# Kernel tuning notes

Measured on AMD Instinct MI355X. Metric: run time of the kernel, lower is better.

The kernel has to match this reference:

```python
import jax, jax.numpy as jnp
import numpy as np

N = 100_000   # nodes
E = 1_600_000 # edges
F_IN = 128
H = 128
C = 16


def setup_inputs() -> dict:
    key = jax.random.key(0)
    ks = jax.random.split(key, 11)
    s = 0.05
    return {
        "x": jax.random.normal(ks[0], (N, F_IN), jnp.float32),
        "edge_index": jax.random.randint(ks[1], (2, E), 0, N, jnp.int32),
        "edge_weight": jax.random.uniform(ks[2], (E,), jnp.float32),
        # first_lin: Linear(features_num, hidden)
        "W_first": jax.random.normal(ks[3], (F_IN, H), jnp.float32) * s,
        "b_first": jax.random.normal(ks[4], (H,), jnp.float32) * s,
        # two GCNConv(hidden, hidden) layers (num_layers - 1 = 2)
        "W_conv1": jax.random.normal(ks[5], (H, H), jnp.float32) * s,
        "b_conv1": jax.random.normal(ks[6], (H,), jnp.float32) * s,
        "W_conv2": jax.random.normal(ks[7], (H, H), jnp.float32) * s,
        "b_conv2": jax.random.normal(ks[8], (H,), jnp.float32) * s,
        # lin2: Linear(hidden, num_class)
        "W_out": jax.random.normal(ks[9], (H, C), jnp.float32) * s,
        "b_out": jax.random.normal(ks[10], (C,), jnp.float32) * s,
    }


def reference(x, edge_index, edge_weight, W_first, b_first,
              W_conv1, b_conv1, W_conv2, b_conv2, W_out, b_out):
    src, dst = edge_index[0], edge_index[1]

    # first_lin + relu (dropout p=0.8 is identity at inference)
    h = jax.nn.relu(x @ W_first + b_first)

    # GCN normalization with self-loops (fill weight 1.0), shared across layers
    deg = jax.ops.segment_sum(edge_weight, dst, num_segments=N) + 1.0
    dinv = jax.lax.rsqrt(deg)                      # [N]
    norm = dinv[src] * edge_weight * dinv[dst]     # [E]
    self_norm = dinv * dinv                        # [N], self-loop contribution

    for W, b in ((W_conv1, b_conv1), (W_conv2, b_conv2)):
        hw = h @ W                                  # [N, H]
        msgs = hw[src] * norm[:, None]              # [E, H] gather + scale
        agg = jax.ops.segment_sum(msgs, dst, num_segments=N)
        agg = agg + hw * self_norm[:, None]         # self-loop term
        h = jax.nn.relu(agg + b)

    # dropout p=0.5 identity at inference; final linear
    return h @ W_out + b_out
```

## Files before the change

### kernel.cpp

```cpp
#include <hip/hip_runtime.h>

typedef unsigned short u16;
typedef unsigned int u32;
using bf16x8 = __attribute__((ext_vector_type(8))) short;
using f32x4  = __attribute__((ext_vector_type(4))) float;

#define SLOT 64
#define RNG 16
#define SPR 4
#define NSHARD 16
#define LDSN 6250
#define CB 256
#define OVF_CAP 65536

static __device__ __forceinline__ u16 f2bf(float f) {
    u32 u = __float_as_uint(f);
    u = (u + 0x7fffu + ((u >> 16) & 1u)) >> 16;
    return (u16)u;
}
static __device__ __forceinline__ float bf2f(u16 h) {
    return __uint_as_float(((u32)h) << 16);
}
static __device__ __forceinline__ float pk_w(u32 e) {
    return (float)(int)((e & 0x7fffu) - 1u) * (1.0f / 32766.0f);
}

__global__ __launch_bounds__(256) void k_part1(const int* __restrict__ dst,
                                               int* __restrict__ cnt, int E, int CH) {
    __shared__ int lc[NSHARD];
    if (threadIdx.x < NSHARD) lc[threadIdx.x] = 0;
    __syncthreads();
    int e0 = blockIdx.x * CH, e1 = min(E, e0 + CH);
    for (int e = e0 + (int)threadIdx.x; e < e1; e += 256)
        atomicAdd(&lc[dst[e] & (NSHARD - 1)], 1);
    __syncthreads();
    if (threadIdx.x < NSHARD) cnt[blockIdx.x * NSHARD + threadIdx.x] = lc[threadIdx.x];
}

__global__ __launch_bounds__(256) void k_scan(const int* __restrict__ cnt,
                                              int* __restrict__ offs, int E) {
    __shared__ int sd[256];
    int t = threadIdx.x;
    int carry = 0;
    for (int base = 0; base < NSHARD * CB; base += 256) {
        int idx = base + t;
        int s = idx / CB, b = idx % CB;
        int v = cnt[b * NSHARD + s];
        sd[t] = v;
        __syncthreads();
        for (int off = 1; off < 256; off <<= 1) {
            int x = (t >= off) ? sd[t - off] : 0;
            __syncthreads();
            sd[t] += x;
            __syncthreads();
        }
        offs[idx] = sd[t] - v + carry;
        carry += sd[255];
        __syncthreads();
    }
    if (t == 0) offs[NSHARD * CB] = E;
}

__global__ __launch_bounds__(256) void k_part2(
    const int* __restrict__ src, const int* __restrict__ dst,
    const float* __restrict__ ew, const int* __restrict__ offs,
    int2* __restrict__ part, int E, int CH) {
    __shared__ int base[NSHARD];
    int t = threadIdx.x, b = blockIdx.x;
    if (t < NSHARD) base[t] = offs[t * CB + b];
    __syncthreads();
    int e0 = b * CH, e1 = min(E, e0 + CH);
    for (int e = e0 + t; e < e1; e += 256) {
        int d = dst[e];
        int s = d & (NSHARD - 1);
        float w = ew[e];
        u32 w15 = 1u + (u32)fminf(w * 32766.0f + 0.5f, 32766.0f);
        u32 ent = ((u32)src[e] << 15) | w15;
        int pos = atomicAdd(&base[s], 1);
        part[pos] = make_int2(d, (int)ent);
    }
}

static __device__ __forceinline__ void fill2_body(
    u32* __restrict__ lcur, int fb, const int2* __restrict__ part,
    const int* __restrict__ offs, u32* __restrict__ bucket,
    int2* __restrict__ ovf, int* __restrict__ ovf_cnt, int E) {
    const int s = fb & (NSHARD - 1);
    const int r = fb >> 4;
    for (int i = threadIdx.x; i < LDSN; i += 256) lcur[i] = 0;
    __syncthreads();
    const int sb = offs[s * CB];
    const int se = offs[(s + 1) * CB];
    const int sz = se - sb;
    const int CHS = (sz + RNG - 1) / RNG;
    const int e0 = sb + r * CHS, e1 = min(se, e0 + CHS);
    for (int e = e0 + (int)threadIdx.x; e < e1; e += 256) {
        int2 v = part[e];
        int d = v.x;
        int ln = d >> 4;
        u32 p = atomicAdd(&lcur[ln], 1u);
        if (p < SPR) {
            bucket[(size_t)d * SLOT + r * SPR + p] = (u32)v.y;
        } else {
            int g = atomicAdd(ovf_cnt, 1);
            if (g < OVF_CAP) ovf[g] = v;
        }
    }
}

__global__ void k_fixup(u32* __restrict__ bucket, const int2* __restrict__ ovf,
                        const int* __restrict__ ovf_cnt) {
    int i = blockIdx.x * blockDim.x + threadIdx.x;
    int c = min(*ovf_cnt, OVF_CAP);
    if (i >= c) return;
    int2 v = ovf[i];
    u32* bp = bucket + (size_t)v.x * SLOT;
    for (int k = 0; k < SLOT; ++k) {
        if (bp[k] == 0u) {
            if (atomicCAS(&bp[k], 0u, (u32)v.y) == 0u) return;
        }
    }
}

static __device__ __forceinline__ void dinv_body(
    const u32* __restrict__ bucket, float* __restrict__ dinv, int n, int db)
{
    int node = db * 16 + (threadIdx.x >> 4);
    if (node >= n) return;
    int l = threadIdx.x & 15;
    const u32* bp = bucket + (size_t)node * SLOT;
    float sum = 0.f;
#pragma unroll
    for (int k = 0; k < 4; ++k) {
        u32 e = bp[l + k * 16];
        if (e) sum += pk_w(e);
    }
    sum += __shfl_xor(sum, 1);
    sum += __shfl_xor(sum, 2);
    sum += __shfl_xor(sum, 4);
    sum += __shfl_xor(sum, 8);
    if (l == 0) dinv[node] = rsqrtf(1.0f + sum);
}

template <bool AF32, bool RELU_BIAS>
static __device__ __forceinline__ void gemm_body(
    u16* __restrict__ Wf, int bid, const void* __restrict__ Araw,
    const float* __restrict__ W, const float* __restrict__ bias,
    u16* __restrict__ C, int n)
{
    const int t = threadIdx.x;
#pragma unroll
    for (int it = 0; it < 8; ++it) {
        int fid = it * 256 + t;
        int c  = fid & 15;
        int g  = (fid >> 4) & 3;
        int kk = (fid >> 6) & 3;
        int ct = fid >> 8;
        int col = ct * 16 + c;
        int k0 = kk * 32 + g * 8;
        const float* wp = W + (size_t)k0 * 128 + col;
        bf16x8 pv;
#pragma unroll
        for (int j = 0; j < 8; ++j) pv[j] = (short)f2bf(wp[(size_t)j * 128]);
        *(bf16x8*)&Wf[(size_t)fid * 8] = pv;
    }
    __syncthreads();

    const int lane = t & 63;
    const int wave = t >> 6;
    const int rowbase = bid * 128 + wave * 32;
    const int lrow = lane & 15;
    const int g = lane >> 4;

    bf16x8 a[2][4];
#pragma unroll
    for (int rt = 0; rt < 2; ++rt) {
        int r = rowbase + rt * 16 + lrow;
        if (r < n) {
            if (AF32) {
                const float* ap = (const float*)Araw + (size_t)r * 128 + g * 8;
#pragma unroll
                for (int kki = 0; kki < 4; ++kki) {
                    float4 v0 = *(const float4*)(ap + kki * 32);
                    float4 v1 = *(const float4*)(ap + kki * 32 + 4);
                    bf16x8 av;
                    av[0] = (short)f2bf(v0.x);
                    av[1] = (short)f2bf(v0.y);
                    av[2] = (short)f2bf(v0.z);
                    av[3] = (short)f2bf(v0.w);
                    av[4] = (short)f2bf(v1.x);
                    av[5] = (short)f2bf(v1.y);
                    av[6] = (short)f2bf(v1.z);
                    av[7] = (short)f2bf(v1.w);
                    a[rt][kki] = av;
                }
            } else {
                const u16* ap = (const u16*)Araw + (size_t)r * 128 + g * 8;
#pragma unroll
                for (int kki = 0; kki < 4; ++kki)
                    a[rt][kki] = *(const bf16x8*)(ap + kki * 32);
            }
        } else {
#pragma unroll
            for (int kki = 0; kki < 4; ++kki)
                a[rt][kki] = (bf16x8)(short)0;
        }
    }

    f32x4 acc[2][8];
#pragma unroll
    for (int rt = 0; rt < 2; ++rt)
#pragma unroll
        for (int ct = 0; ct < 8; ++ct)
            acc[rt][ct] = (f32x4)0.0f;

#pragma unroll
    for (int ct = 0; ct < 8; ++ct) {
#pragma unroll
        for (int kki = 0; kki < 4; ++kki) {
            bf16x8 b = *(const bf16x8*)&Wf[((size_t)(ct * 4 + kki) * 64 + lane) * 8];
            acc[0][ct] = __builtin_amdgcn_mfma_f32_16x16x32_bf16(a[0][kki], b, acc[0][ct], 0, 0, 0);
            acc[1][ct] = __builtin_amdgcn_mfma_f32_16x16x32_bf16(a[1][kki], b, acc[1][ct], 0, 0, 0);
        }
    }

#pragma unroll
    for (int rt = 0; rt < 2; ++rt) {
#pragma unroll
        for (int ct = 0; ct < 8; ++ct) {
            int c = ct * 16 + lrow;
            float bv = 0.f;
            if (RELU_BIAS) bv = bias[c];
#pragma unroll
            for (int j = 0; j < 4; ++j) {
                int r = rowbase + rt * 16 + g * 4 + j;
                if (r < n) {
                    float v = acc[rt][ct][j];
                    if (RELU_BIAS) v = fmaxf(v + bv, 0.f);
                    C[(size_t)r * 128 + c] = f2bf(v);
                }
            }
        }
    }
}

__global__ __launch_bounds__(256) void kC(
    const int2* __restrict__ part, const int* __restrict__ offs,
    u32* __restrict__ bucket, int2* __restrict__ ovf, int* __restrict__ ovf_cnt,
    int E,
    const float* __restrict__ x, const float* __restrict__ W,
    const float* __restrict__ bias, u16* __restrict__ C, int n)
{
    __shared__ u16 Wf[2048 * 8];
    if ((int)blockIdx.x < NSHARD * RNG)
        fill2_body((u32*)Wf, blockIdx.x, part, offs, bucket, ovf, ovf_cnt, E);
    else
        gemm_body<true, true>(Wf, blockIdx.x - NSHARD * RNG, x, W, bias, C, n);
}

__global__ __launch_bounds__(256) void kB(
    const u16* __restrict__ A, const float* __restrict__ W,
    u16* __restrict__ C, int n, int G,
    const u32* __restrict__ bucket, float* __restrict__ dinv)
{
    __shared__ u16 Wf[2048 * 8];
    if ((int)blockIdx.x < G)
        gemm_body<false, false>(Wf, blockIdx.x, A, W, nullptr, C, n);
    else
        dinv_body(bucket, dinv, n, blockIdx.x - G);
}

__global__ __launch_bounds__(256) void k_gemm(
    const u16* __restrict__ A, const float* __restrict__ W,
    u16* __restrict__ C, int n)
{
    __shared__ u16 Wf[2048 * 8];
    gemm_body<false, false>(Wf, blockIdx.x, A, W, nullptr, C, n);
}

__global__ __launch_bounds__(256) void k_gather_fin(
    const u16* __restrict__ hw, const u32* __restrict__ bucket,
    const float* __restrict__ dinv, const float* __restrict__ bias,
    u16* __restrict__ hout, int n)
{
    __shared__ u32 comp[4][64];
    const int w = threadIdx.x >> 6;
    const int lane = threadIdx.x & 63;
    const int node = blockIdx.x * 4 + w;
    const bool active = node < n;

    u32 ent = 0;
    if (active) ent = bucket[(size_t)node * SLOT + lane];
    unsigned long long mask = __ballot(ent != 0);
    int nv = __popcll(mask);
    int pos = __popcll(mask & ((1ull << lane) - 1ull));
    if (ent) comp[w][pos] = ent;
    __syncthreads();
    if (!active) return;

    const int grp = lane >> 4;
    const int gl = lane & 15;
    float acc[8] = {0.f, 0.f, 0.f, 0.f, 0.f, 0.f, 0.f, 0.f};
    int nit = (nv + 3) >> 2;
    int it = 0;
    for (; it + 1 < nit; it += 2) {
        int ka = it * 4 + grp;
        int kb = ka + 4;
        bool vb = kb < nv;
        u32 ea = comp[w][ka];
        u32 eb = comp[w][vb ? kb : 0];
        int sa = (int)(ea >> 15), sb = (int)(eb >> 15);
        bf16x8 ra = *(const bf16x8*)(hw + (size_t)sa * 128 + gl * 8);
        bf16x8 rb = *(const bf16x8*)(hw + (size_t)sb * 128 + gl * 8);
        float wa = dinv[sa] * pk_w(ea);
        float wb = vb ? dinv[sb] * pk_w(eb) : 0.f;
#pragma unroll
        for (int j = 0; j < 8; ++j) acc[j] = fmaf(wa, bf2f((u16)ra[j]), acc[j]);
#pragma unroll
        for (int j = 0; j < 8; ++j) acc[j] = fmaf(wb, bf2f((u16)rb[j]), acc[j]);
    }
    if (it < nit) {
        int ka = it * 4 + grp;
        bool va = ka < nv;
        u32 ea = comp[w][va ? ka : 0];
        int sa = (int)(ea >> 15);
        bf16x8 ra = *(const bf16x8*)(hw + (size_t)sa * 128 + gl * 8);
        float wa = va ? dinv[sa] * pk_w(ea) : 0.f;
#pragma unroll
        for (int j = 0; j < 8; ++j) acc[j] = fmaf(wa, bf2f((u16)ra[j]), acc[j]);
    }
#pragma unroll
    for (int j = 0; j < 8; ++j) {
        acc[j] += __shfl_xor(acc[j], 16);
        acc[j] += __shfl_xor(acc[j], 32);
    }
    if (grp == 0) {
        float di = dinv[node];
        bf16x8 srow = *(const bf16x8*)(hw + (size_t)node * 128 + gl * 8);
        float4 b0 = *(const float4*)(bias + gl * 8);
        float4 b1 = *(const float4*)(bias + gl * 8 + 4);
        float bv[8] = {b0.x, b0.y, b0.z, b0.w, b1.x, b1.y, b1.z, b1.w};
        bf16x8 po;
#pragma unroll
        for (int j = 0; j < 8; ++j) {
            float val = fmaf(di, fmaf(di, bf2f((u16)srow[j]), acc[j]), bv[j]);
            po[j] = (short)f2bf(fmaxf(val, 0.f));
        }
        *(bf16x8*)(hout + (size_t)node * 128 + gl * 8) = po;
    }
}

__global__ void k_gemm_out(const u16* __restrict__ h, const float* __restrict__ W,
                           const float* __restrict__ bias, float* __restrict__ out, int n) {
    __shared__ float hs[16][132];
    __shared__ float wsT[16][132];
    __shared__ float bs[16];
    int t = threadIdx.x;
    int row0 = blockIdx.x * 16;
    int r = t >> 4, c = t & 15;
    {
        int gr = row0 + r;
        if (gr < n) {
            const u16* hp = h + (size_t)gr * 128 + c * 8;
            ushort4 v0 = *(const ushort4*)(hp);
            ushort4 v1 = *(const ushort4*)(hp + 4);
            hs[r][c * 8 + 0] = bf2f(v0.x);
            hs[r][c * 8 + 1] = bf2f(v0.y);
            hs[r][c * 8 + 2] = bf2f(v0.z);
            hs[r][c * 8 + 3] = bf2f(v0.w);
            hs[r][c * 8 + 4] = bf2f(v1.x);
            hs[r][c * 8 + 5] = bf2f(v1.y);
            hs[r][c * 8 + 6] = bf2f(v1.z);
            hs[r][c * 8 + 7] = bf2f(v1.w);
        } else {
#pragma unroll
            for (int j = 0; j < 8; ++j) hs[r][c * 8 + j] = 0.f;
        }
    }
#pragma unroll
    for (int j = 0; j < 8; ++j) {
        int idx = t * 8 + j;
        int k = idx >> 4, cc = idx & 15;
        wsT[cc][k] = W[idx];
    }
    if (t < 16) bs[t] = bias[t];
    __syncthreads();
    float acc = 0.f;
#pragma unroll
    for (int k = 0; k < 128; k += 4) {
        float4 a = *(const float4*)&hs[r][k];
        float4 b = *(const float4*)&wsT[c][k];
        acc += a.x * b.x + a.y * b.y + a.z * b.z + a.w * b.w;
    }
    int gr = row0 + r;
    if (gr < n) out[gr * 16 + c] = acc + bs[c];
}

extern "C" void kernel_launch(void* const* d_in, const int* in_sizes, int n_in,
                              void* d_out, int out_size, void* d_ws, size_t ws_size,
                              hipStream_t stream) {
    const float* x  = (const float*)d_in[0];
    const int*   ei = (const int*)d_in[1];
    const float* ew = (const float*)d_in[2];
    const float* Wf = (const float*)d_in[3];
    const float* bf = (const float*)d_in[4];
    const float* W1 = (const float*)d_in[5];
    const float* b1 = (const float*)d_in[6];
    const float* W2 = (const float*)d_in[7];
    const float* b2 = (const float*)d_in[8];
    const float* Wo = (const float*)d_in[9];
    const float* bo = (const float*)d_in[10];
    float* out = (float*)d_out;

    const int N = in_sizes[0] / 128;
    const int E = in_sizes[2];
    const int* src = ei;
    const int* dst = ei + E;

    char* ws = (char*)d_ws;
    size_t off = 0;
    auto alloc = [&](size_t bytes) -> void* {
        void* p = ws + off;
        off = (off + bytes + 255) & ~(size_t)255;
        return p;
    };
    float* dinv    = (float*)alloc((size_t)N * 4);
    int*   ovf_cnt = (int*)alloc(256);
    int2*  ovf     = (int2*)alloc((size_t)OVF_CAP * 8);
    int*   cnt     = (int*)alloc((size_t)CB * NSHARD * 4);
    int*   offs    = (int*)alloc(((size_t)CB * NSHARD + 1) * 4);
    int2*  part    = (int2*)alloc((size_t)E * 8);
    u32*   bucket  = (u32*)alloc((size_t)N * SLOT * 4);
    u16*   bufA    = (u16*)alloc((size_t)N * 128 * 2);
    u16*   bufB    = (u16*)alloc((size_t)N * 128 * 2);
    (void)ws_size; (void)n_in; (void)out_size;

    const int G  = (N + 127) / 128;
    const int Db = (N + 15) / 16;
    const int gat_grid = (N + 3) / 4;
    const int CH = (E + CB - 1) / CB;

    hipMemsetAsync(bucket, 0, (size_t)N * SLOT * 4, stream);
    hipMemsetAsync(ovf_cnt, 0, 4, stream);

    k_part1<<<CB, 256, 0, stream>>>(dst, cnt, E, CH);
    k_scan<<<1, 256, 0, stream>>>(cnt, offs, E);
    k_part2<<<CB, 256, 0, stream>>>(src, dst, ew, offs, part, E, CH);

    kC<<<NSHARD * RNG + G, 256, 0, stream>>>(part, offs, bucket, ovf, ovf_cnt, E,
                                             x, Wf, bf, bufA, N);
    k_fixup<<<OVF_CAP / 256, 256, 0, stream>>>(bucket, ovf, ovf_cnt);

    kB<<<G + Db, 256, 0, stream>>>(bufA, W1, bufB, N, G, bucket, dinv);
    k_gather_fin<<<gat_grid, 256, 0, stream>>>(bufB, bucket, dinv, b1, bufA, N);
    k_gemm<<<G, 256, 0, stream>>>(bufA, W2, bufB, N);
    k_gather_fin<<<gat_grid, 256, 0, stream>>>(bufB, bucket, dinv, b2, bufA, N);
    k_gemm_out<<<(N + 15) / 16, 256, 0, stream>>>(bufA, Wo, bo, out, N);
}
```

Before: 316.1 us.

## Restructure edge bucketing into LDS-staged shards and fuse output linear into gather

Edge partitioning now uses 128 shards with a two-level parallel scan instead of a single-block scan. Each fill block stages the slot lists in LDS and writes them out as coalesced uint4 stores, which removes the bucket memset and the scattered global writes. The destination shard pass is merged with the first GEMM, and weight fragments are precomputed once in a prep kernel instead of inside every GEMM block. The final 128x16 linear is fused into the second gather kernel, dropping a kernel launch and one full round trip of the hidden activations. The costs are larger LDS use per fill block, a padded bucket layout, and more overflow entries when a node receives more than 16 edges in one quarter.

Result: faster. 269.9 us (-14.6%).

```diff
diff --git a/kernel.cpp b/kernel.cpp
--- a/kernel.cpp
+++ b/kernel.cpp
@@ -6,12 +6,14 @@
 using f32x4  = __attribute__((ext_vector_type(4))) float;
 
 #define SLOT 64
-#define RNG 16
-#define SPR 4
-#define NSHARD 16
-#define LDSN 6250
+#define NSHARD 128
+#define SHMASK 127
+#define SHBITS 7
+#define QRT 4
+#define SPQ 16
+#define LDSN 782
 #define CB 256
-#define OVF_CAP 65536
+#define OVF_CAP 131072
 
 static __device__ __forceinline__ u16 f2bf(float f) {
     u32 u = __float_as_uint(f);
@@ -24,148 +26,77 @@
 static __device__ __forceinline__ float pk_w(u32 e) {
     return (float)(int)((e & 0x7fffu) - 1u) * (1.0f / 32766.0f);
 }
+static __device__ __forceinline__ size_t nodeBase(int d) {
+    return ((size_t)((d & SHMASK) * LDSN + (d >> SHBITS))) << 6;
+}
+
+__global__ void k_prep(const float* __restrict__ Wf, const float* __restrict__ W1,
+                       const float* __restrict__ W2, u16* __restrict__ wfrag) {
+    const float* W = (blockIdx.x == 0) ? Wf : (blockIdx.x == 1 ? W1 : W2);
+    u16* o = wfrag + (size_t)blockIdx.x * 16384;
+    for (int fid = threadIdx.x; fid < 2048; fid += 256) {
+        int c = fid & 15, g = (fid >> 4) & 3, kk = (fid >> 6) & 3, ct = fid >> 8;
+        const float* wp = W + (size_t)(kk * 32 + g * 8) * 128 + ct * 16 + c;
+        bf16x8 pv;
+#pragma unroll
+        for (int j = 0; j < 8; ++j) pv[j] = (short)f2bf(wp[(size_t)j * 128]);
+        *(bf16x8*)&o[(size_t)fid * 8] = pv;
+    }
+}
 
 __global__ __launch_bounds__(256) void k_part1(const int* __restrict__ dst,
                                                int* __restrict__ cnt, int E, int CH) {
     __shared__ int lc[NSHARD];
-    if (threadIdx.x < NSHARD) lc[threadIdx.x] = 0;
+    for (int i = threadIdx.x; i < NSHARD; i += 256) lc[i] = 0;
     __syncthreads();
     int e0 = blockIdx.x * CH, e1 = min(E, e0 + CH);
     for (int e = e0 + (int)threadIdx.x; e < e1; e += 256)
-        atomicAdd(&lc[dst[e] & (NSHARD - 1)], 1);
-    __syncthreads();
-    if (threadIdx.x < NSHARD) cnt[blockIdx.x * NSHARD + threadIdx.x] = lc[threadIdx.x];
-}
-
-__global__ __launch_bounds__(256) void k_scan(const int* __restrict__ cnt,
-                                              int* __restrict__ offs, int E) {
+        atomicAdd(&lc[dst[e] & SHMASK], 1);
+    __syncthreads();
+    for (int i = threadIdx.x; i < NSHARD; i += 256)
+        cnt[blockIdx.x * NSHARD + i] = lc[i];
+}
+
+__global__ __launch_bounds__(256) void k_scan_a(const int* __restrict__ cnt,
+                                                int* __restrict__ offs,
+                                                int* __restrict__ tot) {
     __shared__ int sd[256];
+    int s = blockIdx.x, t = threadIdx.x;
+    int v = cnt[t * NSHARD + s];
+    sd[t] = v;
+    __syncthreads();
+    for (int off = 1; off < 256; off <<= 1) {
+        int x = (t >= off) ? sd[t - off] : 0;
+        __syncthreads();
+        sd[t] += x;
+        __syncthreads();
+    }
+    offs[s * CB + t] = sd[t] - v;
+    if (t == 255) tot[s] = sd[255];
+}
+
+__global__ void k_scan_b(const int* __restrict__ tot, int* __restrict__ base, int E) {
+    __shared__ int sd[NSHARD];
     int t = threadIdx.x;
-    int carry = 0;
-    for (int base = 0; base < NSHARD * CB; base += 256) {
-        int idx = base + t;
-        int s = idx / CB, b = idx % CB;
-        int v = cnt[b * NSHARD + s];
-        sd[t] = v;
+    int v = tot[t];
+    sd[t] = v;
+    __syncthreads();
+    for (int off = 1; off < NSHARD; off <<= 1) {
+        int x = (t >= off) ? sd[t - off] : 0;
         __syncthreads();
-        for (int off = 1; off < 256; off <<= 1) {
-            int x = (t >= off) ? sd[t - off] : 0;
-            __syncthreads();
-            sd[t] += x;
-            __syncthreads();
-        }
-        offs[idx] = sd[t] - v + carry;
-        carry += sd[255];
+        sd[t] += x;
         __syncthreads();
     }
-    if (t == 0) offs[NSHARD * CB] = E;
-}
-
-__global__ __launch_bounds__(256) void k_part2(
-    const int* __restrict__ src, const int* __restrict__ dst,
-    const float* __restrict__ ew, const int* __restrict__ offs,
-    int2* __restrict__ part, int E, int CH) {
-    __shared__ int base[NSHARD];
-    int t = threadIdx.x, b = blockIdx.x;
-    if (t < NSHARD) base[t] = offs[t * CB + b];
-    __syncthreads();
-    int e0 = b * CH, e1 = min(E, e0 + CH);
-    for (int e = e0 + t; e < e1; e += 256) {
-        int d = dst[e];
-        int s = d & (NSHARD - 1);
-        float w = ew[e];
-        u32 w15 = 1u + (u32)fminf(w * 32766.0f + 0.5f, 32766.0f);
-        u32 ent = ((u32)src[e] << 15) | w15;
-        int pos = atomicAdd(&base[s], 1);
-        part[pos] = make_int2(d, (int)ent);
-    }
-}
-
-static __device__ __forceinline__ void fill2_body(
-    u32* __restrict__ lcur, int fb, const int2* __restrict__ part,
-    const int* __restrict__ offs, u32* __restrict__ bucket,
-    int2* __restrict__ ovf, int* __restrict__ ovf_cnt, int E) {
-    const int s = fb & (NSHARD - 1);
-    const int r = fb >> 4;
-    for (int i = threadIdx.x; i < LDSN; i += 256) lcur[i] = 0;
-    __syncthreads();
-    const int sb = offs[s * CB];
-    const int se = offs[(s + 1) * CB];
-    const int sz = se - sb;
-    const int CHS = (sz + RNG - 1) / RNG;
-    const int e0 = sb + r * CHS, e1 = min(se, e0 + CHS);
-    for (int e = e0 + (int)threadIdx.x; e < e1; e += 256) {
-        int2 v = part[e];
-        int d = v.x;
-        int ln = d >> 4;
-        u32 p = atomicAdd(&lcur[ln], 1u);
-        if (p < SPR) {
-            bucket[(size_t)d * SLOT + r * SPR + p] = (u32)v.y;
-        } else {
-            int g = atomicAdd(ovf_cnt, 1);
-            if (g < OVF_CAP) ovf[g] = v;
-        }
-    }
-}
-
-__global__ void k_fixup(u32* __restrict__ bucket, const int2* __restrict__ ovf,
-                        const int* __restrict__ ovf_cnt) {
-    int i = blockIdx.x * blockDim.x + threadIdx.x;
-    int c = min(*ovf_cnt, OVF_CAP);
-    if (i >= c) return;
-    int2 v = ovf[i];
-    u32* bp = bucket + (size_t)v.x * SLOT;
-    for (int k = 0; k < SLOT; ++k) {
-        if (bp[k] == 0u) {
-            if (atomicCAS(&bp[k], 0u, (u32)v.y) == 0u) return;
-        }
-    }
-}
-
-static __device__ __forceinline__ void dinv_body(
-    const u32* __restrict__ bucket, float* __restrict__ dinv, int n, int db)
-{
-    int node = db * 16 + (threadIdx.x >> 4);
-    if (node >= n) return;
-    int l = threadIdx.x & 15;
-    const u32* bp = bucket + (size_t)node * SLOT;
-    float sum = 0.f;
-#pragma unroll
-    for (int k = 0; k < 4; ++k) {
-        u32 e = bp[l + k * 16];
-        if (e) sum += pk_w(e);
-    }
-    sum += __shfl_xor(sum, 1);
-    sum += __shfl_xor(sum, 2);
-    sum += __shfl_xor(sum, 4);
-    sum += __shfl_xor(sum, 8);
-    if (l == 0) dinv[node] = rsqrtf(1.0f + sum);
+    base[t] = sd[t] - v;
+    if (t == NSHARD - 1) base[NSHARD] = E;
 }
 
 template <bool AF32, bool RELU_BIAS>
 static __device__ __forceinline__ void gemm_body(
-    u16* __restrict__ Wf, int bid, const void* __restrict__ Araw,
-    const float* __restrict__ W, const float* __restrict__ bias,
-    u16* __restrict__ C, int n)
+    int bid, const void* __restrict__ Araw, const u16* __restrict__ Wfrag,
+    const float* __restrict__ bias, u16* __restrict__ C, int n)
 {
     const int t = threadIdx.x;
-#pragma unroll
-    for (int it = 0; it < 8; ++it) {
-        int fid = it * 256 + t;
-        int c  = fid & 15;
-        int g  = (fid >> 4) & 3;
-        int kk = (fid >> 6) & 3;
-        int ct = fid >> 8;
-        int col = ct * 16 + c;
-        int k0 = kk * 32 + g * 8;
-        const float* wp = W + (size_t)k0 * 128 + col;
-        bf16x8 pv;
-#pragma unroll
-        for (int j = 0; j < 8; ++j) pv[j] = (short)f2bf(wp[(size_t)j * 128]);
-        *(bf16x8*)&Wf[(size_t)fid * 8] = pv;
-    }
-    __syncthreads();
-
     const int lane = t & 63;
     const int wave = t >> 6;
     const int rowbase = bid * 128 + wave * 32;
@@ -218,7 +149,7 @@
     for (int ct = 0; ct < 8; ++ct) {
 #pragma unroll
         for (int kki = 0; kki < 4; ++kki) {
-            bf16x8 b = *(const bf16x8*)&Wf[((size_t)(ct * 4 + kki) * 64 + lane) * 8];
+            bf16x8 b = *(const bf16x8*)&Wfrag[((size_t)(ct * 4 + kki) * 64 + lane) * 8];
             acc[0][ct] = __builtin_amdgcn_mfma_f32_16x16x32_bf16(a[0][kki], b, acc[0][ct], 0, 0, 0);
             acc[1][ct] = __builtin_amdgcn_mfma_f32_16x16x32_bf16(a[1][kki], b, acc[1][ct], 0, 0, 0);
         }
@@ -244,53 +175,144 @@
     }
 }
 
-__global__ __launch_bounds__(256) void kC(
-    const int2* __restrict__ part, const int* __restrict__ offs,
+__global__ __launch_bounds__(256) void kD(
+    const int* __restrict__ src, const int* __restrict__ dst,
+    const float* __restrict__ ew, const int* __restrict__ offs,
+    const int* __restrict__ base, int2* __restrict__ part, int E, int CH,
+    const float* __restrict__ x, const u16* __restrict__ wfragF,
+    const float* __restrict__ bias, u16* __restrict__ C, int n)
+{
+    __shared__ int sbase[NSHARD];
+    if ((int)blockIdx.x < CB) {
+        int b = blockIdx.x, t = threadIdx.x;
+        for (int i = t; i < NSHARD; i += 256) sbase[i] = base[i] + offs[i * CB + b];
+        __syncthreads();
+        int e0 = b * CH, e1 = min(E, e0 + CH);
+        for (int e = e0 + t; e < e1; e += 256) {
+            int d = dst[e];
+            float w = ew[e];
+            u32 w15 = 1u + (u32)fminf(w * 32766.0f + 0.5f, 32766.0f);
+            u32 ent = ((u32)src[e] << 15) | w15;
+            int pos = atomicAdd(&sbase[d & SHMASK], 1);
+            part[pos] = make_int2(d, (int)ent);
+        }
+    } else {
+        gemm_body<true, true>(blockIdx.x - CB, x, wfragF, bias, C, n);
+    }
+}
+
+__global__ __launch_bounds__(256) void k_fill3(
+    const int2* __restrict__ part, const int* __restrict__ base,
     u32* __restrict__ bucket, int2* __restrict__ ovf, int* __restrict__ ovf_cnt,
-    int E,
-    const float* __restrict__ x, const float* __restrict__ W,
-    const float* __restrict__ bias, u16* __restrict__ C, int n)
-{
-    __shared__ u16 Wf[2048 * 8];
-    if ((int)blockIdx.x < NSHARD * RNG)
-        fill2_body((u32*)Wf, blockIdx.x, part, offs, bucket, ovf, ovf_cnt, E);
-    else
-        gemm_body<true, true>(Wf, blockIdx.x - NSHARD * RNG, x, W, bias, C, n);
+    int n)
+{
+    __shared__ u32 slots[LDSN * SPQ];
+    __shared__ u32 cur[LDSN];
+    const int s = blockIdx.x >> 2;
+    const int q = blockIdx.x & 3;
+    for (int i = threadIdx.x; i < LDSN * SPQ; i += 256) slots[i] = 0;
+    for (int i = threadIdx.x; i < LDSN; i += 256) cur[i] = 0;
+    __syncthreads();
+    const int rb = base[s], re = base[s + 1];
+    const int CHS = (re - rb + 3) >> 2;
+    const int e0 = rb + q * CHS, e1 = min(re, e0 + CHS);
+    for (int e = e0 + (int)threadIdx.x; e < e1; e += 256) {
+        int2 v = part[e];
+        int ln = v.x >> SHBITS;
+        u32 p = atomicAdd(&cur[ln], 1u);
+        if (p < SPQ) {
+            slots[ln * SPQ + p] = (u32)v.y;
+        } else {
+            int g2 = atomicAdd(ovf_cnt, 1);
+            if (g2 < OVF_CAP) ovf[g2] = v;
+        }
+    }
+    __syncthreads();
+    for (int i = threadIdx.x; i < LDSN * 4; i += 256) {
+        int ln = i >> 2, k = i & 3;
+        int d = (ln << SHBITS) + s;
+        if (d < n) {
+            u32* dp = bucket + nodeBase(d) + q * SPQ + k * 4;
+            *(uint4*)dp = *(const uint4*)&slots[ln * SPQ + k * 4];
+        }
+    }
+}
+
+__global__ void k_fixup(u32* __restrict__ bucket, const int2* __restrict__ ovf,
+                        const int* __restrict__ ovf_cnt) {
+    int i = blockIdx.x * blockDim.x + threadIdx.x;
+    int c = min(*ovf_cnt, OVF_CAP);
+    if (i >= c) return;
+    int2 v = ovf[i];
+    u32* bp = bucket + nodeBase(v.x);
+    for (int k = 0; k < SLOT; ++k) {
+        if (bp[k] == 0u) {
+            if (atomicCAS(&bp[k], 0u, (u32)v.y) == 0u) return;
+        }
+    }
+}
+
+static __device__ __forceinline__ void dinv_body(
+    const u32* __restrict__ bucket, float* __restrict__ dinv, int n, int db)
+{
+    int node = db * 16 + (threadIdx.x >> 4);
+    if (node >= n) return;
+    int l = threadIdx.x & 15;
+    const u32* bp = bucket + nodeBase(node);
+    float sum = 0.f;
+#pragma unroll
+    for (int k = 0; k < 4; ++k) {
+        u32 e = bp[l + k * 16];
+        if (e) sum += pk_w(e);
+    }
+    sum += __shfl_xor(sum, 1);
+    sum += __shfl_xor(sum, 2);
+    sum += __shfl_xor(sum, 4);
+    sum += __shfl_xor(sum, 8);
+    if (l == 0) dinv[node] = rsqrtf(1.0f + sum);
 }
 
 __global__ __launch_bounds__(256) void kB(
-    const u16* __restrict__ A, const float* __restrict__ W,
+    const u16* __restrict__ A, const u16* __restrict__ wfrag1,
     u16* __restrict__ C, int n, int G,
     const u32* __restrict__ bucket, float* __restrict__ dinv)
 {
-    __shared__ u16 Wf[2048 * 8];
     if ((int)blockIdx.x < G)
-        gemm_body<false, false>(Wf, blockIdx.x, A, W, nullptr, C, n);
+        gemm_body<false, false>(blockIdx.x, A, wfrag1, nullptr, C, n);
     else
         dinv_body(bucket, dinv, n, blockIdx.x - G);
 }
 
 __global__ __launch_bounds__(256) void k_gemm(
-    const u16* __restrict__ A, const float* __restrict__ W,
+    const u16* __restrict__ A, const u16* __restrict__ wfrag,
     u16* __restrict__ C, int n)
 {
-    __shared__ u16 Wf[2048 * 8];
-    gemm_body<false, false>(Wf, blockIdx.x, A, W, nullptr, C, n);
-}
-
+    gemm_body<false, false>(blockIdx.x, A, wfrag, nullptr, C, n);
+}
+
+template <bool FINAL>
 __global__ __launch_bounds__(256) void k_gather_fin(
     const u16* __restrict__ hw, const u32* __restrict__ bucket,
     const float* __restrict__ dinv, const float* __restrict__ bias,
-    u16* __restrict__ hout, int n)
+    u16* __restrict__ hout,
+    const float* __restrict__ Wo, const float* __restrict__ bo,
+    float* __restrict__ out, int n)
 {
     __shared__ u32 comp[4][64];
+    __shared__ float WoS[FINAL ? 2048 : 1];
+    __shared__ float bos[FINAL ? 16 : 1];
     const int w = threadIdx.x >> 6;
     const int lane = threadIdx.x & 63;
     const int node = blockIdx.x * 4 + w;
     const bool active = node < n;
 
+    if (FINAL) {
+        for (int i = threadIdx.x; i < 2048; i += 256) WoS[i] = Wo[i];
+        if (threadIdx.x < 16) bos[threadIdx.x] = bo[threadIdx.x];
+    }
+
     u32 ent = 0;
-    if (active) ent = bucket[(size_t)node * SLOT + lane];
+    if (active) ent = bucket[nodeBase(node) + lane];
     unsigned long long mask = __ballot(ent != 0);
     int nv = __popcll(mask);
     int pos = __popcll(mask & ((1ull << lane) - 1ull));
@@ -334,66 +356,36 @@
         acc[j] += __shfl_xor(acc[j], 16);
         acc[j] += __shfl_xor(acc[j], 32);
     }
-    if (grp == 0) {
-        float di = dinv[node];
-        bf16x8 srow = *(const bf16x8*)(hw + (size_t)node * 128 + gl * 8);
-        float4 b0 = *(const float4*)(bias + gl * 8);
-        float4 b1 = *(const float4*)(bias + gl * 8 + 4);
-        float bv[8] = {b0.x, b0.y, b0.z, b0.w, b1.x, b1.y, b1.z, b1.w};
-        bf16x8 po;
-#pragma unroll
-        for (int j = 0; j < 8; ++j) {
-            float val = fmaf(di, fmaf(di, bf2f((u16)srow[j]), acc[j]), bv[j]);
-            po[j] = (short)f2bf(fmaxf(val, 0.f));
-        }
-        *(bf16x8*)(hout + (size_t)node * 128 + gl * 8) = po;
-    }
-}
-
-__global__ void k_gemm_out(const u16* __restrict__ h, const float* __restrict__ W,
-                           const float* __restrict__ bias, float* __restrict__ out, int n) {
-    __shared__ float hs[16][132];
-    __shared__ float wsT[16][132];
-    __shared__ float bs[16];
-    int t = threadIdx.x;
-    int row0 = blockIdx.x * 16;
-    int r = t >> 4, c = t & 15;
-    {
-        int gr = row0 + r;
-        if (gr < n) {
-            const u16* hp = h + (size_t)gr * 128 + c * 8;
-            ushort4 v0 = *(const ushort4*)(hp);
-            ushort4 v1 = *(const ushort4*)(hp + 4);
-            hs[r][c * 8 + 0] = bf2f(v0.x);
-            hs[r][c * 8 + 1] = bf2f(v0.y);
-            hs[r][c * 8 + 2] = bf2f(v0.z);
-            hs[r][c * 8 + 3] = bf2f(v0.w);
-            hs[r][c * 8 + 4] = bf2f(v1.x);
-            hs[r][c * 8 + 5] = bf2f(v1.y);
-            hs[r][c * 8 + 6] = bf2f(v1.z);
-            hs[r][c * 8 + 7] = bf2f(v1.w);
-        } else {
-#pragma unroll
-            for (int j = 0; j < 8; ++j) hs[r][c * 8 + j] = 0.f;
-        }
-    }
-#pragma unroll
-    for (int j = 0; j < 8; ++j) {
-        int idx = t * 8 + j;
-        int k = idx >> 4, cc = idx & 15;
-        wsT[cc][k] = W[idx];
-    }
-    if (t < 16) bs[t] = bias[t];
-    __syncthreads();
-    float acc = 0.f;
-#pragma unroll
-    for (int k = 0; k < 128; k += 4) {
-        float4 a = *(const float4*)&hs[r][k];
-        float4 b = *(const float4*)&wsT[c][k];
-        acc += a.x * b.x + a.y * b.y + a.z * b.z + a.w * b.w;
-    }
-    int gr = row0 + r;
-    if (gr < n) out[gr * 16 + c] = acc + bs[c];
+
+    float di = dinv[node];
+    bf16x8 srow = *(const bf16x8*)(hw + (size_t)node * 128 + gl * 8);
+    float4 b0 = *(const float4*)(bias + gl * 8);
+    float4 b1 = *(const float4*)(bias + gl * 8 + 4);
+    float bv[8] = {b0.x, b0.y, b0.z, b0.w, b1.x, b1.y, b1.z, b1.w};
+    float hfin[8];
+#pragma unroll
+    for (int j = 0; j < 8; ++j)
+        hfin[j] = fmaxf(fmaf(di, fmaf(di, bf2f((u16)srow[j]), acc[j]), bv[j]), 0.f);
+
+    if (!FINAL) {
+        if (grp == 0) {
+            bf16x8 po;
+#pragma unroll
+            for (int j = 0; j < 8; ++j) po[j] = (short)f2bf(hfin[j]);
+            *(bf16x8*)(hout + (size_t)node * 128 + gl * 8) = po;
+        }
+    } else {
+        float partial = 0.f;
+#pragma unroll
+        for (int jj = 0; jj < 32; ++jj) {
+            int j = grp * 32 + jj;
+            float hj = __shfl(hfin[jj & 7], j >> 3);
+            partial = fmaf(hj, WoS[j * 16 + gl], partial);
+        }
+        partial += __shfl_xor(partial, 16);
+        partial += __shfl_xor(partial, 32);
+        if (grp == 0) out[(size_t)node * 16 + gl] = partial + bos[gl];
+    }
 }
 
 extern "C" void kernel_launch(void* const* d_in, const int* in_sizes, int n_in,
@@ -428,9 +420,12 @@
     int*   ovf_cnt = (int*)alloc(256);
     int2*  ovf     = (int2*)alloc((size_t)OVF_CAP * 8);
     int*   cnt     = (int*)alloc((size_t)CB * NSHARD * 4);
-    int*   offs    = (int*)alloc(((size_t)CB * NSHARD + 1) * 4);
+    int*   offs    = (int*)alloc((size_t)NSHARD * CB * 4);
+    int*   tot     = (int*)alloc((size_t)NSHARD * 4);
+    int*   base    = (int*)alloc((size_t)(NSHARD + 1) * 4);
+    u16*   wfrag   = (u16*)alloc((size_t)3 * 16384 * 2);
     int2*  part    = (int2*)alloc((size_t)E * 8);
-    u32*   bucket  = (u32*)alloc((size_t)N * SLOT * 4);
+    u32*   bucket  = (u32*)alloc((size_t)NSHARD * LDSN * SLOT * 4);
     u16*   bufA    = (u16*)alloc((size_t)N * 128 * 2);
     u16*   bufB    = (u16*)alloc((size_t)N * 128 * 2);
     (void)ws_size; (void)n_in; (void)out_size;
@@ -440,20 +435,20 @@
     const int gat_grid = (N + 3) / 4;
     const int CH = (E + CB - 1) / CB;
 
-    hipMemsetAsync(bucket, 0, (size_t)N * SLOT * 4, stream);
     hipMemsetAsync(ovf_cnt, 0, 4, stream);
 
+    k_prep<<<3, 256, 0, stream>>>(Wf, W1, W2, wfrag);
     k_part1<<<CB, 256, 0, stream>>>(dst, cnt, E, CH);
-    k_scan<<<1, 256, 0, stream>>>(cnt, offs, E);
-    k_part2<<<CB, 256, 0, stream>>>(src, dst, ew, offs, part, E, CH);
-
-    kC<<<NSHARD * RNG + G, 256, 0, stream>>>(part, offs, bucket, ovf, ovf_cnt, E,
-                                             x, Wf, bf, bufA, N);
+    k_scan_a<<<NSHARD, 256, 0, stream>>>(cnt, offs, tot);
+    k_scan_b<<<1, NSHARD, 0, stream>>>(tot, base, E);
+    kD<<<CB + G, 256, 0, stream>>>(src, dst, ew, offs, base, part, E, CH,
+                                   x, wfrag, bf, bufA, N);
+    k_fill3<<<NSHARD * QRT, 256, 0, stream>>>(part, base, bucket, ovf, ovf_cnt, N);
     k_fixup<<<OVF_CAP / 256, 256, 0, stream>>>(bucket, ovf, ovf_cnt);
-
-    kB<<<G + Db, 256, 0, stream>>>(bufA, W1, bufB, N, G, bucket, dinv);
-    k_gather_fin<<<gat_grid, 256, 0, stream>>>(bufB, bucket, dinv, b1, bufA, N);
-    k_gemm<<<G, 256, 0, stream>>>(bufA, W2, bufB, N);
-    k_gather_fin<<<gat_grid, 256, 0, stream>>>(bufB, bucket, dinv, b2, bufA, N);
-    k_gemm_out<<<(N + 15) / 16, 256, 0, stream>>>(bufA, Wo, bo, out, N);
-}
+    kB<<<G + Db, 256, 0, stream>>>(bufA, wfrag + 16384, bufB, N, G, bucket, dinv);
+    k_gather_fin<false><<<gat_grid, 256, 0, stream>>>(bufB, bucket, dinv, b1, bufA,
+                                                      nullptr, nullptr, nullptr, N);
+    k_gemm<<<G, 256, 0, stream>>>(bufA, wfrag + 32768, bufB, N);
+    k_gather_fin<true><<<gat_grid, 256, 0, stream>>>(bufB, bucket, dinv, b2, nullptr,
+                                                     Wo, bo, out, N);
+}
```
